# Performance work log

Hardware: AMD Instinct MI355X
Metric: run time of the kernel (lower is better)

## Reference

```python
import jax, jax.numpy as jnp
import numpy as np

E, H, O = 64, 128, 16  # enc_hidden_dim, dec_hidden_dim, dec_output_dim (proj_size)
B, N, FUT = 64, 1000, 12


def _lstm_proj_cell(x, h, c, W_ih, W_hh, b_ih, b_hh, W_hr):
    # PyTorch gate order: input, forget, cell(g), output
    gates = x @ W_ih.T + h @ W_hh.T + (b_ih + b_hh)
    i, f, g, o = jnp.split(gates, 4, axis=-1)
    c_new = jax.nn.sigmoid(f) * c + jax.nn.sigmoid(i) * jnp.tanh(g)
    h_full = jax.nn.sigmoid(o) * jnp.tanh(c_new)
    h_new = h_full @ W_hr.T  # proj_size projection
    return h_new, c_new


def setup_inputs() -> dict:
    key = jax.random.key(0)
    ks = jax.random.split(key, 20)
    sc = 0.1
    inp = {
        "enc_outputs": jax.random.normal(ks[0], (B, 1, N, E), jnp.float32),
        "mean": jax.random.normal(ks[1], (B, FUT, N, O), jnp.float32),
        "s": jax.random.normal(ks[2], (1, O), jnp.float32),
        "h_0": jax.random.normal(ks[3], (2, O), jnp.float32),
        "c_0": jax.random.normal(ks[4], (2, H), jnp.float32),
        "W_ih_l0": sc * jax.random.normal(ks[5], (4 * H, E + O), jnp.float32),
        "W_hh_l0": sc * jax.random.normal(ks[6], (4 * H, O), jnp.float32),
        "b_ih_l0": sc * jax.random.normal(ks[7], (4 * H,), jnp.float32),
        "b_hh_l0": sc * jax.random.normal(ks[8], (4 * H,), jnp.float32),
        "W_hr_l0": sc * jax.random.normal(ks[9], (O, H), jnp.float32),
        "W_ih_l1": sc * jax.random.normal(ks[10], (4 * H, O), jnp.float32),
        "W_hh_l1": sc * jax.random.normal(ks[11], (4 * H, O), jnp.float32),
        "b_ih_l1": sc * jax.random.normal(ks[12], (4 * H,), jnp.float32),
        "b_hh_l1": sc * jax.random.normal(ks[13], (4 * H,), jnp.float32),
        "W_hr_l1": sc * jax.random.normal(ks[14], (O, H), jnp.float32),
        "future": FUT,
    }
    # forget-gate bias = 1.0 as in reset_bias()
    for nme in ("b_ih_l0", "b_hh_l0", "b_ih_l1", "b_hh_l1"):
        inp[nme] = inp[nme].at[H:2 * H].set(1.0)
    return inp


def _forward(enc_outputs, mean, s, h_0, c_0,
             W_ih_l0, W_hh_l0, b_ih_l0, b_hh_l0, W_hr_l0,
             W_ih_l1, W_hh_l1, b_ih_l1, b_hh_l1, W_hr_l1, future):
    b, _, n_nodes, _ = enc_outputs.shape
    enc = enc_outputs[:, 0]            # [B, N, E]
    node_mean = jnp.mean(mean, axis=1)  # [B, N, O]
    # state is carried across nodes AND timesteps: one chain of N*future steps
    node_idx = jnp.arange(n_nodes * future) // future

    last0 = jnp.broadcast_to(s[0], (b, s.shape[1]))
    h1_0 = jnp.broadcast_to(h_0[0], (b, h_0.shape[1]))
    h2_0 = jnp.broadcast_to(h_0[1], (b, h_0.shape[1]))
    c1_0 = jnp.broadcast_to(c_0[0], (b, c_0.shape[1]))
    c2_0 = jnp.broadcast_to(c_0[1], (b, c_0.shape[1]))

    def step(carry, n):
        last, h1, c1, h2, c2 = carry
        enc_t = jnp.take(enc, n, axis=1)        # [B, E]
        nm_t = jnp.take(node_mean, n, axis=1)   # [B, O]
        loop = last + nm_t                      # TFRate forced to 0.0 in source
        x = jnp.concatenate([enc_t, loop], axis=-1)
        h1, c1 = _lstm_proj_cell(x, h1, c1, W_ih_l0, W_hh_l0, b_ih_l0, b_hh_l0, W_hr_l0)
        h2, c2 = _lstm_proj_cell(h1, h2, c2, W_ih_l1, W_hh_l1, b_ih_l1, b_hh_l1, W_hr_l1)
        return (h2, h1, c1, h2, c2), h2 + nm_t

    _, outs = jax.lax.scan(step, (last0, h1_0, c1_0, h2_0, c2_0), node_idx)
    # outs: [N*future, B, O] -> [B, future, N, O]
    outs = outs.reshape(n_nodes, future, b, -1).transpose(2, 1, 0, 3)
    return outs


def reference(enc_outputs, mean, s, h_0, c_0,
              W_ih_l0, W_hh_l0, b_ih_l0, b_hh_l0, W_hr_l0,
              W_ih_l1, W_hh_l1, b_ih_l1, b_hh_l1, W_hr_l1, future):
    return _forward(enc_outputs, mean, s, h_0, c_0,
                    W_ih_l0, W_hh_l0, b_ih_l0, b_hh_l0, W_hr_l0,
                    W_ih_l1, W_hh_l1, b_ih_l1, b_hh_l1, W_hr_l1, future)
```

## Files before the change

kernel.cpp:

```cpp
#include <hip/hip_runtime.h>

#define BB 64
#define NN 1000
#define FF 12
#define EE 64
#define HH 128
#define OO 16

__device__ __forceinline__ float rcp_(float x){ return __builtin_amdgcn_rcpf(x); }
__device__ __forceinline__ float sigm_(float x){ return rcp_(1.0f + __expf(-x)); }
__device__ __forceinline__ float tanh_(float x){ return 1.0f - 2.0f*rcp_(__expf(2.0f*x) + 1.0f); }

__global__ __launch_bounds__(256, 1)
void decoder_kernel(const float* __restrict__ enc,
                    const float* __restrict__ mean,
                    const float* __restrict__ sv,
                    const float* __restrict__ h0,
                    const float* __restrict__ c0,
                    const float* __restrict__ Wih0,
                    const float* __restrict__ Whh0,
                    const float* __restrict__ bih0,
                    const float* __restrict__ bhh0,
                    const float* __restrict__ Whr0,
                    const float* __restrict__ Wih1,
                    const float* __restrict__ Whh1,
                    const float* __restrict__ bih1,
                    const float* __restrict__ bhh1,
                    const float* __restrict__ Whr1,
                    float* __restrict__ out)
{
    const int t = threadIdx.x;
    const int b = blockIdx.x;

    const int u  = t >> 1;
    const int m  = t & 1;
    const int rA = m*HH + u;
    const int rB = m*HH + 2*HH + u;

    const int j16 = t >> 4;
    const int kq  = t & 15;
    const int kc  = kq * 8;

    __shared__ __align__(16) float s_hfull[HH];
    __shared__ __align__(16) float s_h1[OO];
    __shared__ __align__(16) float s_h2[OO];
    __shared__ __align__(16) float s_last[OO];
    __shared__ __align__(16) float s_enc[EE];
    __shared__ __align__(16) float s_nm[OO];

    float wAe[EE], wBe[EE];
    float wAl[OO], wBl[OO];
    float wAh[OO], wBh[OO];
    float w1Ai[OO], w1Bi[OO];
    float w1Ah[OO], w1Bh[OO];
    {
        const float* ra = Wih0 + (size_t)rA*(EE+OO);
        const float* rb = Wih0 + (size_t)rB*(EE+OO);
        #pragma unroll
        for (int e=0;e<EE;e++){ wAe[e]=ra[e]; wBe[e]=rb[e]; }
        #pragma unroll
        for (int j=0;j<OO;j++){ wAl[j]=ra[EE+j]; wBl[j]=rb[EE+j]; }
        #pragma unroll
        for (int j=0;j<OO;j++){ wAh[j]=Whh0[rA*OO+j]; wBh[j]=Whh0[rB*OO+j]; }
        #pragma unroll
        for (int j=0;j<OO;j++){ w1Ai[j]=Wih1[rA*OO+j]; w1Bi[j]=Wih1[rB*OO+j]; }
        #pragma unroll
        for (int j=0;j<OO;j++){ w1Ah[j]=Whh1[rA*OO+j]; w1Bh[j]=Whh1[rB*OO+j]; }
    }
    const float b0A = bih0[rA] + bhh0[rA];
    const float b0B = bih0[rB] + bhh0[rB];
    const float b1A = bih1[rA] + bhh1[rA];
    const float b1B = bih1[rB] + bhh1[rB];

    float wp0[8], wp1[8];
    #pragma unroll
    for (int k=0;k<8;k++){
        wp0[k] = Whr0[j16*HH + kc + k];
        wp1[k] = Whr1[j16*HH + kc + k];
    }

    float c1u = c0[u];
    float c2u = c0[HH + u];

    if (t < OO){
        s_last[t] = sv[t];
        s_h1[t]   = h0[t];
        s_h2[t]   = h0[OO + t];
    }

    const float* encB  = enc  + (size_t)b * NN * EE;
    const float* meanB = mean + (size_t)b * FF * NN * OO;
    float*       outB  = out  + (size_t)b * FF * NN * OO;

    float4 pf_enc = make_float4(0.f,0.f,0.f,0.f);
    float  pf_nm[FF];
    if (t < 16){
        pf_enc = ((const float4*)encB)[t];
    } else if (t < 32){
        const int j = t - 16;
        #pragma unroll
        for (int ff=0; ff<FF; ++ff) pf_nm[ff] = meanB[(ff*NN + 0)*OO + j];
    }
    __syncthreads();

    for (int n = 0; n < NN; ++n){
        if (t < 16){
            ((float4*)s_enc)[t] = pf_enc;
        } else if (t < 32){
            float a = 0.0f;
            #pragma unroll
            for (int ff=0; ff<FF; ++ff) a += pf_nm[ff];
            s_nm[t-16] = a * (1.0f/12.0f);
        }
        __syncthreads();

        const int n1 = (n+1 < NN) ? (n+1) : n;
        if (t < 16){
            pf_enc = ((const float4*)encB)[n1*16 + t];
        } else if (t < 32){
            const int j = t - 16;
            #pragma unroll
            for (int ff=0; ff<FF; ++ff) pf_nm[ff] = meanB[(ff*NN + n1)*OO + j];
        }

        float preA = b0A, preB = b0B;
        #pragma unroll
        for (int e=0;e<EE;e++){ const float ev = s_enc[e]; preA += ev*wAe[e]; preB += ev*wBe[e]; }
        #pragma unroll
        for (int j=0;j<OO;j++){ const float nv = s_nm[j]; preA += nv*wAl[j]; preB += nv*wBl[j]; }
        const float nmj = s_nm[j16];

        #pragma unroll 1
        for (int f = 0; f < FF; ++f){
            {
                float aA = preA, aB = preB;
                #pragma unroll
                for (int j=0;j<OO;j++){ const float lv = s_last[j]; aA += lv*wAl[j]; aB += lv*wBl[j]; }
                #pragma unroll
                for (int j=0;j<OO;j++){ const float hv = s_h1[j];   aA += hv*wAh[j]; aB += hv*wBh[j]; }
                const float gA = sigm_(aA);
                const float gB = (m==0) ? tanh_(aB) : sigm_(aB);
                const float sendv = (m==0) ? gA*gB : gA;
                const float recvv = __shfl_xor(sendv, 1, 64);
                const float Fv   = (m==0) ? recvv : sendv;
                const float prod = (m==0) ? sendv : recvv;
                c1u = Fv*c1u + prod;
                if (m==1) s_hfull[u] = gB * tanh_(c1u);
            }
            __syncthreads();

            {
                const float4 ha = *(const float4*)&s_hfull[kc];
                const float4 hb = *(const float4*)&s_hfull[kc+4];
                float p = ha.x*wp0[0] + ha.y*wp0[1] + ha.z*wp0[2] + ha.w*wp0[3]
                        + hb.x*wp0[4] + hb.y*wp0[5] + hb.z*wp0[6] + hb.w*wp0[7];
                p += __shfl_xor(p, 8, 64);
                p += __shfl_xor(p, 4, 64);
                p += __shfl_xor(p, 2, 64);
                p += __shfl_xor(p, 1, 64);
                if (kq == 0) s_h1[j16] = p;
            }
            __syncthreads();

            {
                float aA = b1A, aB = b1B;
                #pragma unroll
                for (int j=0;j<OO;j++){ const float hv = s_h1[j]; aA += hv*w1Ai[j]; aB += hv*w1Bi[j]; }
                #pragma unroll
                for (int j=0;j<OO;j++){ const float hv = s_h2[j]; aA += hv*w1Ah[j]; aB += hv*w1Bh[j]; }
                const float gA = sigm_(aA);
                const float gB = (m==0) ? tanh_(aB) : sigm_(aB);
                const float sendv = (m==0) ? gA*gB : gA;
                const float recvv = __shfl_xor(sendv, 1, 64);
                const float Fv   = (m==0) ? recvv : sendv;
                const float prod = (m==0) ? sendv : recvv;
                c2u = Fv*c2u + prod;
                if (m==1) s_hfull[u] = gB * tanh_(c2u);
            }
            __syncthreads();

            {
                const float4 ha = *(const float4*)&s_hfull[kc];
                const float4 hb = *(const float4*)&s_hfull[kc+4];
                float p = ha.x*wp1[0] + ha.y*wp1[1] + ha.z*wp1[2] + ha.w*wp1[3]
                        + hb.x*wp1[4] + hb.y*wp1[5] + hb.z*wp1[6] + hb.w*wp1[7];
                p += __shfl_xor(p, 8, 64);
                p += __shfl_xor(p, 4, 64);
                p += __shfl_xor(p, 2, 64);
                p += __shfl_xor(p, 1, 64);
                if (kq == 0){
                    s_h2[j16]   = p;
                    s_last[j16] = p;
                    outB[(f*NN + n)*OO + j16] = p + nmj;
                }
            }
            __syncthreads();
        }
    }
}

extern "C" void kernel_launch(void* const* d_in, const int* in_sizes, int n_in,
                              void* d_out, int out_size, void* d_ws, size_t ws_size,
                              hipStream_t stream) {
    const float* enc  = (const float*)d_in[0];
    const float* mean = (const float*)d_in[1];
    const float* sv   = (const float*)d_in[2];
    const float* h0   = (const float*)d_in[3];
    const float* c0   = (const float*)d_in[4];
    const float* Wih0 = (const float*)d_in[5];
    const float* Whh0 = (const float*)d_in[6];
    const float* bih0 = (const float*)d_in[7];
    const float* bhh0 = (const float*)d_in[8];
    const float* Whr0 = (const float*)d_in[9];
    const float* Wih1 = (const float*)d_in[10];
    const float* Whh1 = (const float*)d_in[11];
    const float* bih1 = (const float*)d_in[12];
    const float* bhh1 = (const float*)d_in[13];
    const float* Whr1 = (const float*)d_in[14];
    float* out = (float*)d_out;

    decoder_kernel<<<dim3(BB), dim3(256), 0, stream>>>(
        enc, mean, sv, h0, c0,
        Wih0, Whh0, bih0, bhh0, Whr0,
        Wih1, Whh1, bih1, bhh1, Whr1,
        out);
}
```

Baseline: 16.14 ms.

## Vectorize LSTM dot products, shrink projection to one wave, batch output stores

Reworks the per-step recurrences to use float4 accumulators with four independent partial sums, which shortens the dependent FMA chains. The hidden projection now runs redundantly in every wave over a padded shared buffer with a 4-lane reduction instead of 16 lanes. Outputs are staged in shared memory and written once per node as float4 stores rather than as scalar stores on each timestep. The enc part of W_ih0 is no longer held in registers and is read from global memory for every node, which cuts register pressure but adds global loads that are likely served from cache.

```diff
diff --git a/kernel.cpp b/kernel.cpp
--- a/kernel.cpp
+++ b/kernel.cpp
@@ -10,6 +10,11 @@
 __device__ __forceinline__ float rcp_(float x){ return __builtin_amdgcn_rcpf(x); }
 __device__ __forceinline__ float sigm_(float x){ return rcp_(1.0f + __expf(-x)); }
 __device__ __forceinline__ float tanh_(float x){ return 1.0f - 2.0f*rcp_(__expf(2.0f*x) + 1.0f); }
+
+__device__ __forceinline__ float4 fma4(float4 a, float4 x, float4 w){
+    a.x += x.x*w.x; a.y += x.y*w.y; a.z += x.z*w.z; a.w += x.w*w.w; return a;
+}
+__device__ __forceinline__ float hsum4(float4 a){ return (a.x+a.y)+(a.z+a.w); }
 
 __global__ __launch_bounds__(256, 1)
 void decoder_kernel(const float* __restrict__ enc,
@@ -35,48 +40,43 @@
     const int u  = t >> 1;
     const int m  = t & 1;
     const int rA = m*HH + u;
-    const int rB = m*HH + 2*HH + u;
-
-    const int j16 = t >> 4;
-    const int kq  = t & 15;
-    const int kc  = kq * 8;
-
-    __shared__ __align__(16) float s_hfull[HH];
+    const int rB = rA + 2*HH;
+
+    const int lane = t & 63;
+    const int j16  = lane >> 2;
+    const int q    = lane & 3;
+
+    __shared__ __align__(16) float s_last[OO];
     __shared__ __align__(16) float s_h1[OO];
     __shared__ __align__(16) float s_h2[OO];
-    __shared__ __align__(16) float s_last[OO];
     __shared__ __align__(16) float s_enc[EE];
     __shared__ __align__(16) float s_nm[OO];
-
-    float wAe[EE], wBe[EE];
-    float wAl[OO], wBl[OO];
-    float wAh[OO], wBh[OO];
-    float w1Ai[OO], w1Bi[OO];
-    float w1Ah[OO], w1Bh[OO];
-    {
-        const float* ra = Wih0 + (size_t)rA*(EE+OO);
-        const float* rb = Wih0 + (size_t)rB*(EE+OO);
-        #pragma unroll
-        for (int e=0;e<EE;e++){ wAe[e]=ra[e]; wBe[e]=rb[e]; }
-        #pragma unroll
-        for (int j=0;j<OO;j++){ wAl[j]=ra[EE+j]; wBl[j]=rb[EE+j]; }
-        #pragma unroll
-        for (int j=0;j<OO;j++){ wAh[j]=Whh0[rA*OO+j]; wBh[j]=Whh0[rB*OO+j]; }
-        #pragma unroll
-        for (int j=0;j<OO;j++){ w1Ai[j]=Wih1[rA*OO+j]; w1Bi[j]=Wih1[rB*OO+j]; }
-        #pragma unroll
-        for (int j=0;j<OO;j++){ w1Ah[j]=Whh1[rA*OO+j]; w1Bh[j]=Whh1[rB*OO+j]; }
+    __shared__ __align__(16) float s_hf[4*36];
+    __shared__ __align__(16) float s_out[FF*OO];
+
+    float4 wAl[4], wBl[4], wAh[4], wBh[4];
+    float4 w1Ai[4], w1Bi[4], w1Ah[4], w1Bh[4];
+    #pragma unroll
+    for (int k=0;k<4;k++){
+        wAl[k]  = *(const float4*)&Wih0[(size_t)rA*(EE+OO) + EE + 4*k];
+        wBl[k]  = *(const float4*)&Wih0[(size_t)rB*(EE+OO) + EE + 4*k];
+        wAh[k]  = *(const float4*)&Whh0[rA*OO + 4*k];
+        wBh[k]  = *(const float4*)&Whh0[rB*OO + 4*k];
+        w1Ai[k] = *(const float4*)&Wih1[rA*OO + 4*k];
+        w1Bi[k] = *(const float4*)&Wih1[rB*OO + 4*k];
+        w1Ah[k] = *(const float4*)&Whh1[rA*OO + 4*k];
+        w1Bh[k] = *(const float4*)&Whh1[rB*OO + 4*k];
     }
     const float b0A = bih0[rA] + bhh0[rA];
     const float b0B = bih0[rB] + bhh0[rB];
     const float b1A = bih1[rA] + bhh1[rA];
     const float b1B = bih1[rB] + bhh1[rB];
 
-    float wp0[8], wp1[8];
+    float4 wp0[8], wp1[8];
     #pragma unroll
-    for (int k=0;k<8;k++){
-        wp0[k] = Whr0[j16*HH + kc + k];
-        wp1[k] = Whr1[j16*HH + kc + k];
+    for (int i=0;i<8;i++){
+        wp0[i] = *(const float4*)&Whr0[j16*HH + q*32 + 4*i];
+        wp1[i] = *(const float4*)&Whr1[j16*HH + q*32 + 4*i];
     }
 
     float c1u = c0[u];
@@ -92,25 +92,27 @@
     const float* meanB = mean + (size_t)b * FF * NN * OO;
     float*       outB  = out  + (size_t)b * FF * NN * OO;
 
-    float4 pf_enc = make_float4(0.f,0.f,0.f,0.f);
+    const float4* wrowA = (const float4*)(Wih0 + (size_t)rA*(EE+OO));
+    const float4* wrowB = (const float4*)(Wih0 + (size_t)rB*(EE+OO));
+
+    float4 pf_enc = make_float4(0,0,0,0);
     float  pf_nm[FF];
     if (t < 16){
         pf_enc = ((const float4*)encB)[t];
     } else if (t < 32){
         const int j = t - 16;
         #pragma unroll
-        for (int ff=0; ff<FF; ++ff) pf_nm[ff] = meanB[(ff*NN + 0)*OO + j];
-    }
-    __syncthreads();
+        for (int ff=0; ff<FF; ++ff) pf_nm[ff] = meanB[(size_t)(ff*NN)*OO + j];
+    }
 
     for (int n = 0; n < NN; ++n){
         if (t < 16){
             ((float4*)s_enc)[t] = pf_enc;
         } else if (t < 32){
-            float a = 0.0f;
-            #pragma unroll
-            for (int ff=0; ff<FF; ++ff) a += pf_nm[ff];
-            s_nm[t-16] = a * (1.0f/12.0f);
+            float a0 = pf_nm[0]+pf_nm[4], a1 = pf_nm[1]+pf_nm[5];
+            float a2 = pf_nm[2]+pf_nm[6], a3 = pf_nm[3]+pf_nm[7];
+            a0 += pf_nm[8]; a1 += pf_nm[9]; a2 += pf_nm[10]; a3 += pf_nm[11];
+            s_nm[t-16] = ((a0+a1)+(a2+a3)) * (1.0f/12.0f);
         }
         __syncthreads();
 
@@ -120,81 +122,116 @@
         } else if (t < 32){
             const int j = t - 16;
             #pragma unroll
-            for (int ff=0; ff<FF; ++ff) pf_nm[ff] = meanB[(ff*NN + n1)*OO + j];
-        }
-
-        float preA = b0A, preB = b0B;
-        #pragma unroll
-        for (int e=0;e<EE;e++){ const float ev = s_enc[e]; preA += ev*wAe[e]; preB += ev*wBe[e]; }
-        #pragma unroll
-        for (int j=0;j<OO;j++){ const float nv = s_nm[j]; preA += nv*wAl[j]; preB += nv*wBl[j]; }
+            for (int ff=0; ff<FF; ++ff) pf_nm[ff] = meanB[(size_t)(ff*NN + n1)*OO + j];
+        }
+
+        float preA, preB;
+        {
+            float4 sa = make_float4(b0A, 0.f, 0.f, 0.f);
+            float4 sb = make_float4(b0B, 0.f, 0.f, 0.f);
+            #pragma unroll
+            for (int k=0;k<16;k++){
+                const float4 e = ((const float4*)s_enc)[k];
+                sa = fma4(sa, e, wrowA[k]);
+                sb = fma4(sb, e, wrowB[k]);
+            }
+            float4 nm4[4];
+            #pragma unroll
+            for (int k=0;k<4;k++) nm4[k] = ((const float4*)s_nm)[k];
+            #pragma unroll
+            for (int k=0;k<4;k++){ sa = fma4(sa, nm4[k], wAl[k]); sb = fma4(sb, nm4[k], wBl[k]); }
+            preA = hsum4(sa);
+            preB = hsum4(sb);
+        }
         const float nmj = s_nm[j16];
 
         #pragma unroll 1
         for (int f = 0; f < FF; ++f){
             {
-                float aA = preA, aB = preB;
-                #pragma unroll
-                for (int j=0;j<OO;j++){ const float lv = s_last[j]; aA += lv*wAl[j]; aB += lv*wBl[j]; }
-                #pragma unroll
-                for (int j=0;j<OO;j++){ const float hv = s_h1[j];   aA += hv*wAh[j]; aB += hv*wBh[j]; }
+                float4 L[4], H[4];
+                #pragma unroll
+                for (int k=0;k<4;k++){ L[k] = ((const float4*)s_last)[k]; H[k] = ((const float4*)s_h1)[k]; }
+                float4 accA = make_float4(preA, 0.f, 0.f, 0.f);
+                float4 accB = make_float4(preB, 0.f, 0.f, 0.f);
+                #pragma unroll
+                for (int k=0;k<4;k++){
+                    accA = fma4(accA, L[k], wAl[k]); accA = fma4(accA, H[k], wAh[k]);
+                    accB = fma4(accB, L[k], wBl[k]); accB = fma4(accB, H[k], wBh[k]);
+                }
+                const float aA = hsum4(accA);
+                const float aB = hsum4(accB);
                 const float gA = sigm_(aA);
                 const float gB = (m==0) ? tanh_(aB) : sigm_(aB);
                 const float sendv = (m==0) ? gA*gB : gA;
                 const float recvv = __shfl_xor(sendv, 1, 64);
-                const float Fv   = (m==0) ? recvv : sendv;
-                const float prod = (m==0) ? sendv : recvv;
+                const float Fv    = (m==0) ? recvv : sendv;
+                const float prod  = (m==0) ? sendv : recvv;
                 c1u = Fv*c1u + prod;
-                if (m==1) s_hfull[u] = gB * tanh_(c1u);
-            }
-            __syncthreads();
-
-            {
-                const float4 ha = *(const float4*)&s_hfull[kc];
-                const float4 hb = *(const float4*)&s_hfull[kc+4];
-                float p = ha.x*wp0[0] + ha.y*wp0[1] + ha.z*wp0[2] + ha.w*wp0[3]
-                        + hb.x*wp0[4] + hb.y*wp0[5] + hb.z*wp0[6] + hb.w*wp0[7];
-                p += __shfl_xor(p, 8, 64);
-                p += __shfl_xor(p, 4, 64);
+                if (m) s_hf[u + ((u>>5)<<2)] = gB * tanh_(c1u);
+            }
+            __syncthreads();
+
+            {
+                float4 acc = make_float4(0.f,0.f,0.f,0.f);
+                #pragma unroll
+                for (int i=0;i<8;i++){
+                    const float4 h = *(const float4*)&s_hf[q*36 + 4*i];
+                    acc = fma4(acc, h, wp0[i]);
+                }
+                float p = hsum4(acc);
+                p += __shfl_xor(p, 1, 64);
                 p += __shfl_xor(p, 2, 64);
-                p += __shfl_xor(p, 1, 64);
-                if (kq == 0) s_h1[j16] = p;
-            }
-            __syncthreads();
-
-            {
-                float aA = b1A, aB = b1B;
-                #pragma unroll
-                for (int j=0;j<OO;j++){ const float hv = s_h1[j]; aA += hv*w1Ai[j]; aB += hv*w1Bi[j]; }
-                #pragma unroll
-                for (int j=0;j<OO;j++){ const float hv = s_h2[j]; aA += hv*w1Ah[j]; aB += hv*w1Bh[j]; }
+                if (t < 64 && q == 0) s_h1[j16] = p;
+            }
+            __syncthreads();
+
+            {
+                float4 X[4], H[4];
+                #pragma unroll
+                for (int k=0;k<4;k++){ X[k] = ((const float4*)s_h1)[k]; H[k] = ((const float4*)s_h2)[k]; }
+                float4 accA = make_float4(b1A, 0.f, 0.f, 0.f);
+                float4 accB = make_float4(b1B, 0.f, 0.f, 0.f);
+                #pragma unroll
+                for (int k=0;k<4;k++){
+                    accA = fma4(accA, X[k], w1Ai[k]); accA = fma4(accA, H[k], w1Ah[k]);
+                    accB = fma4(accB, X[k], w1Bi[k]); accB = fma4(accB, H[k], w1Bh[k]);
+                }
+                const float aA = hsum4(accA);
+                const float aB = hsum4(accB);
                 const float gA = sigm_(aA);
                 const float gB = (m==0) ? tanh_(aB) : sigm_(aB);
                 const float sendv = (m==0) ? gA*gB : gA;
                 const float recvv = __shfl_xor(sendv, 1, 64);
-                const float Fv   = (m==0) ? recvv : sendv;
-                const float prod = (m==0) ? sendv : recvv;
+                const float Fv    = (m==0) ? recvv : sendv;
+                const float prod  = (m==0) ? sendv : recvv;
                 c2u = Fv*c2u + prod;
-                if (m==1) s_hfull[u] = gB * tanh_(c2u);
-            }
-            __syncthreads();
-
-            {
-                const float4 ha = *(const float4*)&s_hfull[kc];
-                const float4 hb = *(const float4*)&s_hfull[kc+4];
-                float p = ha.x*wp1[0] + ha.y*wp1[1] + ha.z*wp1[2] + ha.w*wp1[3]
-                        + hb.x*wp1[4] + hb.y*wp1[5] + hb.z*wp1[6] + hb.w*wp1[7];
-                p += __shfl_xor(p, 8, 64);
-                p += __shfl_xor(p, 4, 64);
+                if (m) s_hf[u + ((u>>5)<<2)] = gB * tanh_(c2u);
+            }
+            __syncthreads();
+
+            {
+                float4 acc = make_float4(0.f,0.f,0.f,0.f);
+                #pragma unroll
+                for (int i=0;i<8;i++){
+                    const float4 h = *(const float4*)&s_hf[q*36 + 4*i];
+                    acc = fma4(acc, h, wp1[i]);
+                }
+                float p = hsum4(acc);
+                p += __shfl_xor(p, 1, 64);
                 p += __shfl_xor(p, 2, 64);
-                p += __shfl_xor(p, 1, 64);
-                if (kq == 0){
+                if (t < 64 && q == 0){
                     s_h2[j16]   = p;
                     s_last[j16] = p;
-                    outB[(f*NN + n)*OO + j16] = p + nmj;
-                }
-            }
-            __syncthreads();
+                    s_out[f*OO + j16] = p + nmj;
+                }
+            }
+            __syncthreads();
+        }
+
+        if (t < 48){
+            const int ff = t >> 2, o4 = (t & 3) * 4;
+            const float4 v = *(const float4*)&s_out[ff*OO + o4];
+            *(float4*)&outB[(size_t)(ff*NN + n)*OO + o4] = v;
         }
     }
 }
```

After: 17.08 ms. 5.8% more time.
